# Kernel tuning notes

Hardware: AMD Instinct MI355X
Metric: run time of the kernel (lower is better)

Reference implementation:

```python
import jax, jax.numpy as jnp
import numpy as np

ATOM, BOND, INNER, HID, REC, OHID = 14, 3, 20, 34, 20, 25
N_NODES = 1048576
N_EDGES = 983040
MAX_DEPTH = 16
N_GRAPHS = 16384


def leaky(x):
    return jnp.where(x >= 0, x, 0.01 * x)


def setup_inputs() -> dict:
    key = jax.random.key(0)
    ks = jax.random.split(key, 20)
    p = 0.02
    atom_feats = jax.random.normal(ks[0], (N_NODES, ATOM), jnp.float32)
    bond_feats = jax.random.normal(ks[1], (N_EDGES, BOND), jnp.float32)
    # build a forest: node i's parent is some node with strictly smaller depth.
    # For a jit-friendly synthetic instance we assign depths and connect each
    # non-root node (edge) from a parent at depth d to child at depth d+1.
    depth = np.asarray(jax.random.randint(ks[2], (N_NODES,), 0, MAX_DEPTH))
    order = np.argsort(depth, kind='stable')
    depth_sorted = depth[order]
    # edges: child must have depth >= 1; pick children among nodes with depth>0
    child_pool = order[depth_sorted > 0]
    rng = np.random.default_rng(0)
    child_idx = rng.choice(child_pool, size=N_EDGES, replace=False) if len(child_pool) >= N_EDGES else rng.choice(child_pool, size=N_EDGES, replace=True)
    child_depth = depth[child_idx]
    # parent: random node with depth == child_depth - 1
    # bucket nodes by depth
    buckets = [order[depth_sorted == d] for d in range(MAX_DEPTH)]
    parent_idx = np.empty(N_EDGES, dtype=np.int64)
    for d in range(1, MAX_DEPTH):
        m = child_depth == d
        if m.sum() > 0:
            parent_idx[m] = rng.choice(buckets[d - 1], size=int(m.sum()))
    graph_id = np.asarray(jax.random.randint(ks[3], (N_NODES,), 0, N_GRAPHS))
    # roots: nodes with no incoming edge (not a child)
    is_child = np.zeros(N_NODES, dtype=bool)
    is_child[child_idx] = True
    is_root = (~is_child).astype(np.float32)
    params = {
        'inner_w': jax.random.normal(ks[4], (REC + BOND, INNER), jnp.float32) * p,
        'inner_b': jnp.zeros((INNER,), jnp.float32),
        'net_w1': jax.random.normal(ks[5], (INNER + ATOM, HID), jnp.float32) * p,
        'net_b1': jnp.zeros((HID,), jnp.float32),
        'net_w2': jax.random.normal(ks[6], (HID, REC), jnp.float32) * p,
        'net_b2': jnp.zeros((REC,), jnp.float32),
        'net0_w1': jax.random.normal(ks[7], (ATOM, HID), jnp.float32) * p,
        'net0_b1': jnp.zeros((HID,), jnp.float32),
        'net0_w2': jax.random.normal(ks[8], (HID, REC), jnp.float32) * p,
        'net0_b2': jnp.zeros((REC,), jnp.float32),
        'out_w1': jax.random.normal(ks[9], (REC, OHID), jnp.float32) * p,
        'out_b1': jnp.zeros((OHID,), jnp.float32),
        'out_w2': jax.random.normal(ks[10], (OHID, 1), jnp.float32) * p,
        'out_b2': jnp.zeros((1,), jnp.float32),
    }
    return dict(atom_feats=atom_feats, bond_feats=bond_feats,
                parent_idx=jnp.asarray(parent_idx), child_idx=jnp.asarray(child_idx),
                node_depth=jnp.asarray(depth), graph_id=jnp.asarray(graph_id),
                is_root=jnp.asarray(is_root), **params)


def reference(atom_feats, bond_feats, parent_idx, child_idx, node_depth, graph_id,
              is_root, inner_w, inner_b, net_w1, net_b1, net_w2, net_b2,
              net0_w1, net0_b1, net0_w2, net0_b2, out_w1, out_b1, out_w2, out_b2):
    n_nodes = atom_feats.shape[0]
    has_child = jnp.zeros((n_nodes,), jnp.float32).at[parent_idx].add(1.0) > 0
    # leaf vector via net0
    leaf_vec = leaky(leaky(atom_feats @ net0_w1 + net0_b1) @ net0_w2 + net0_b2)  # [N, REC]
    h = leaf_vec  # node recursive vectors; internal nodes filled bottom-up
    # process depths from deepest-1 parents up to 0: at step d, update nodes at depth d
    for d in range(MAX_DEPTH - 2, -1, -1):
        child_h = h[child_idx]  # [E, REC]
        msg = leaky(jnp.concatenate([bond_feats, child_h], axis=1) @ inner_w + inner_b)  # [E, INNER]
        # only edges whose parent is at depth d contribute this step
        edge_mask = (node_depth[parent_idx] == d).astype(msg.dtype)[:, None]
        inner_sum = jnp.zeros((n_nodes, INNER), msg.dtype).at[parent_idx].add(msg * edge_mask)
        x = jnp.concatenate([atom_feats, inner_sum], axis=1)  # [N, ATOM+INNER]
        new_h = leaky(leaky(x @ net_w1 + net_b1) @ net_w2 + net_b2)
        upd = ((node_depth == d) & has_child).astype(h.dtype)[:, None]
        h = h * (1.0 - upd) + new_h * upd
    # sum root vectors per graph
    root_h = h * is_root[:, None]
    g = jax.ops.segment_sum(root_h, graph_id, num_segments=N_GRAPHS)  # [G, REC]
    out = jnp.tanh(g @ out_w1 + out_b1) @ out_w2 + out_b2  # [G, 1]
    return out.reshape(-1)
```

## Files before the change

kernel.cpp:

```cpp
#include <hip/hip_runtime.h>

#define ATOM  14
#define BOND  3
#define INNER 20
#define HID   34
#define HIDP  36
#define REC   20
#define OHID  25
#define NN    1048576
#define NE    983040
#define NG    16384

#define NB    512
#define NT    256
#define GT    (NB*NT)
#define NIT   (NN/GT)

#define NB2   1024
#define NT2   256
#define NGRP  (NT2/4)
#define SSTR  (NGRP+1)
#define NBINS (NB2*32)

__device__ __forceinline__ float leaky(float x) { return x >= 0.f ? x : 0.01f * x; }

__device__ __forceinline__ void wsync() {
    __builtin_amdgcn_wave_barrier();
    __builtin_amdgcn_sched_barrier(0);
}

__device__ __forceinline__ void gbar_f(int* bar, int goal) {
    __syncthreads();
    if (threadIdx.x == 0) {
        __threadfence();
        __hip_atomic_fetch_add(bar, 1, __ATOMIC_RELEASE, __HIP_MEMORY_SCOPE_AGENT);
        while (__hip_atomic_load(bar, __ATOMIC_RELAXED, __HIP_MEMORY_SCOPE_AGENT) < goal)
            __builtin_amdgcn_s_sleep(32);
        __threadfence();
    }
    __syncthreads();
}

__global__ void k_pre(int* cnt_n, int2* pnode2, float* g, int* bin_cnt, int* totals, int* bars) {
    int tid = blockIdx.x * 256 + threadIdx.x;
    for (int i = tid; i < NN; i += 262144) { cnt_n[i] = 0; pnode2[i] = make_int2(i, -1); }
    for (int i = tid; i < NG * REC; i += 262144) g[i] = 0.f;
    for (int i = tid; i < NBINS; i += 262144) bin_cnt[i] = 0;
    if (tid == 0) { totals[0] = 0; totals[16] = 0; }
    if (tid == 1) for (int k = 0; k < 32; ++k) bars[k] = 0;
}

__global__ __launch_bounds__(NT) void k_prep(
    const int* __restrict__ parent, const int* __restrict__ child,
    const int* __restrict__ depth, const int* __restrict__ gid,
    const float* __restrict__ isr,
    int* cnt_n, int2* pnode2, int* K_s,
    int4* nodeinfo, int* row_n, int* adjc,
    int* bin_cnt, int* bin_base, int* bin_cur,
    int* totals, int* bar)
{
    __shared__ int sh[NT];
    __shared__ int sbase_sh;
    const int t = threadIdx.x;
    const int tid = blockIdx.x * NT + t;
    int ep = 0;

    for (int e = tid; e < NE; e += GT) {
        int p = parent[e];
        int r = atomicAdd(&cnt_n[p], 1);
        pnode2[child[e]] = make_int2(p, (r << 20) | e);
    }
    gbar_f(bar, NB * ++ep);

    for (int i = tid; i < NN; i += GT) {
        int d = depth[i];
        int r = i;
        for (int s = 0; s < d; ++s) r = pnode2[r].x;
        int K = (r & (NB2 - 1)) * 32 + d * 2 + (cnt_n[i] == 0 ? 1 : 0);
        K_s[i] = K;
        atomicAdd(&bin_cnt[K], 1);
    }
    gbar_f(bar, NB * ++ep);

    if (blockIdx.x < NBINS / NT) {
        int k0 = blockIdx.x * NT + t;
        int v = bin_cnt[k0];
        sh[t] = v;
        __syncthreads();
        for (int ofs = 1; ofs < NT; ofs <<= 1) {
            int x = (t >= ofs) ? sh[t - ofs] : 0;
            __syncthreads();
            sh[t] += x;
            __syncthreads();
        }
        if (t == NT - 1) sbase_sh = atomicAdd(&totals[0], sh[t]);
        __syncthreads();
        int b = sbase_sh + sh[t] - v;
        bin_base[k0] = b;
        bin_cur[k0] = b;
    }
    gbar_f(bar, NB * ++ep);

    for (int k = 0; k < NIT; ++k) {
        int i = tid + k * GT;
        int cn = cnt_n[i];
        __syncthreads();
        sh[t] = cn;
        __syncthreads();
        for (int ofs = 1; ofs < NT; ofs <<= 1) {
            int x = (t >= ofs) ? sh[t - ofs] : 0;
            __syncthreads();
            sh[t] += x;
            __syncthreads();
        }
        if (t == NT - 1) sbase_sh = atomicAdd(&totals[16], sh[t]);
        __syncthreads();
        int row = sbase_sh + sh[t] - cn;
        int pos = atomicAdd(&bin_cur[K_s[i]], 1);
        int2 pe = pnode2[i];
        int gr = (isr[i] != 0.f) ? gid[i] : -1;
        nodeinfo[pos] = make_int4(i, pe.y, gr, (row << 12) | cn);
        row_n[i] = row;
    }
    gbar_f(bar, NB * ++ep);

    for (int pos = tid; pos < NN; pos += GT) {
        int4 ni = nodeinfo[pos];
        if (ni.z < 0) {
            int ppn = pnode2[ni.x].x;
            int rank = ((unsigned)ni.y) >> 20;
            int slot = row_n[ppn] + rank;
            adjc[slot] = pos;
        }
    }
}

__device__ __forceinline__ void coop_mlp(int slot, int j, int KN,
                                         const float* xs, float* hs, float* os,
                                         const float* w1, const float* b1,
                                         const float* w2, const float* b2,
                                         float* o)
{
    wsync();
    float acc[9];
    #pragma unroll
    for (int u = 0; u < 9; ++u) { int h = 9*j + u; acc[u] = (h < HID) ? b1[h] : 0.f; }
    #pragma unroll 2
    for (int k = 0; k < KN; ++k) {
        float xk = xs[k * SSTR + slot];
        #pragma unroll
        for (int u = 0; u < 9; ++u) { int h = 9*j + u; if (h < HID) acc[u] += xk * w1[k * HIDP + h]; }
    }
    #pragma unroll
    for (int u = 0; u < 9; ++u) { int h = 9*j + u; if (h < HID) hs[h * SSTR + slot] = leaky(acc[u]); }
    wsync();
    #pragma unroll
    for (int u = 0; u < 5; ++u) o[u] = b2[5*j + u];
    #pragma unroll 2
    for (int k = 0; k < HID; ++k) {
        float hk = hs[k * SSTR + slot];
        #pragma unroll
        for (int u = 0; u < 5; ++u) o[u] += hk * w2[k * REC + 5*j + u];
    }
    #pragma unroll
    for (int u = 0; u < 5; ++u) { o[u] = leaky(o[u]); os[(5*j + u) * SSTR + slot] = o[u]; }
    wsync();
}

__global__ __launch_bounds__(NT2) void k_levels(
    const float* __restrict__ atom, const float* __restrict__ bond,
    const int4* __restrict__ nodeinfo, const int* __restrict__ adjc,
    const int* __restrict__ bin_base, const int* __restrict__ bin_cnt,
    const float* __restrict__ iw, const float* __restrict__ ib,
    const float* __restrict__ nw1, const float* __restrict__ nb1,
    const float* __restrict__ nw2, const float* __restrict__ nb2,
    const float* __restrict__ l0w1, const float* __restrict__ l0b1,
    const float* __restrict__ l0w2, const float* __restrict__ l0b2,
    float* __restrict__ g, float* __restrict__ msg_s)
{
    __shared__ float lw1[34 * HIDP];
    __shared__ float lw2[HID * REC];
    __shared__ float liw[23 * REC];
    __shared__ float zw1[ATOM * HIDP];
    __shared__ float zw2[HID * REC];
    __shared__ float lb1[HID], lb2[REC], lbi[INNER], zb1[HID], zb2[REC];
    __shared__ float xs[34 * SSTR];
    __shared__ float hs[34 * SSTR];
    __shared__ float os[20 * SSTR];

    const int t = threadIdx.x;
    const int b = blockIdx.x;
    const int slot = t >> 2;
    const int j = t & 3;

    for (int idx = t; idx < 34 * HIDP; idx += NT2) {
        int r = idx / HIDP, c = idx - r * HIDP;
        lw1[idx] = (c < HID) ? nw1[r * HID + c] : 0.f;
    }
    for (int idx = t; idx < HID * REC; idx += NT2) { lw2[idx] = nw2[idx]; zw2[idx] = l0w2[idx]; }
    for (int idx = t; idx < 23 * REC; idx += NT2) liw[idx] = iw[idx];
    for (int idx = t; idx < ATOM * HIDP; idx += NT2) {
        int r = idx / HIDP, c = idx - r * HIDP;
        zw1[idx] = (c < HID) ? l0w1[r * HID + c] : 0.f;
    }
    if (t < HID) { lb1[t] = nb1[t]; zb1[t] = l0b1[t]; }
    else if (t >= 64 && t < 64 + REC) { lb2[t - 64] = nb2[t - 64]; zb2[t - 64] = l0b2[t - 64]; }
    if (t >= 96 && t < 96 + INNER) lbi[t - 96] = ib[t - 96];
    __syncthreads();

    for (int d = 15; d >= 0; --d) {
        {
            int K = b * 32 + d * 2;
            int base = bin_base[K], n0 = bin_cnt[K];
            for (int idx = slot; idx < n0; idx += NGRP) {
                int pos = base + idx;
                int4 ni = nodeinfo[pos];
                int n   = ni.w & 0xFFF;
                int rp0 = ((unsigned)ni.w) >> 12;
                float s0 = 0.f, s1 = 0.f, s2 = 0.f, s3 = 0.f, s4 = 0.f;
                for (int r = rp0; r < rp0 + n; ++r) {
                    const float* mp = msg_s + (size_t)adjc[r] * REC + 5*j;
                    s0 += mp[0]; s1 += mp[1]; s2 += mp[2]; s3 += mp[3]; s4 += mp[4];
                }
                const float* ar = atom + (size_t)ni.x * ATOM;
                #pragma unroll
                for (int u = 0; u < 4; ++u) { int k = 4*j + u; if (k < ATOM) xs[k * SSTR + slot] = ar[k]; }
                xs[(ATOM + 5*j + 0) * SSTR + slot] = s0;
                xs[(ATOM + 5*j + 1) * SSTR + slot] = s1;
                xs[(ATOM + 5*j + 2) * SSTR + slot] = s2;
                xs[(ATOM + 5*j + 3) * SSTR + slot] = s3;
                xs[(ATOM + 5*j + 4) * SSTR + slot] = s4;
                float o[5];
                coop_mlp(slot, j, ATOM + INNER, xs, hs, os, lw1, lb1, lw2, lb2, o);
                if (ni.z >= 0) {
                    #pragma unroll
                    for (int u = 0; u < 5; ++u) atomicAdd(&g[(size_t)ni.z * REC + 5*j + u], o[u]);
                } else {
                    const float* br = bond + (size_t)(ni.y & 0xFFFFF) * BOND;
                    float b0 = br[0], b1 = br[1], b2 = br[2];
                    float m[5];
                    #pragma unroll
                    for (int u = 0; u < 5; ++u)
                        m[u] = lbi[5*j + u] + b0 * liw[0 * INNER + 5*j + u]
                             + b1 * liw[1 * INNER + 5*j + u] + b2 * liw[2 * INNER + 5*j + u];
                    #pragma unroll 2
                    for (int k = 0; k < REC; ++k) {
                        float ok = os[k * SSTR + slot];
                        #pragma unroll
                        for (int u = 0; u < 5; ++u) m[u] += ok * liw[(BOND + k) * INNER + 5*j + u];
                    }
                    #pragma unroll
                    for (int u = 0; u < 5; ++u) msg_s[(size_t)pos * REC + 5*j + u] = leaky(m[u]);
                }
            }
        }
        {
            int K = b * 32 + d * 2 + 1;
            int base = bin_base[K], n1 = bin_cnt[K];
            for (int idx = slot; idx < n1; idx += NGRP) {
                int pos = base + idx;
                int4 ni = nodeinfo[pos];
                const float* ar = atom + (size_t)ni.x * ATOM;
                #pragma unroll
                for (int u = 0; u < 4; ++u) { int k = 4*j + u; if (k < ATOM) xs[k * SSTR + slot] = ar[k]; }
                float o[5];
                coop_mlp(slot, j, ATOM, xs, hs, os, zw1, zb1, zw2, zb2, o);
                if (ni.z >= 0) {
                    #pragma unroll
                    for (int u = 0; u < 5; ++u) atomicAdd(&g[(size_t)ni.z * REC + 5*j + u], o[u]);
                } else {
                    const float* br = bond + (size_t)(ni.y & 0xFFFFF) * BOND;
                    float b0 = br[0], b1 = br[1], b2 = br[2];
                    float m[5];
                    #pragma unroll
                    for (int u = 0; u < 5; ++u)
                        m[u] = lbi[5*j + u] + b0 * liw[0 * INNER + 5*j + u]
                             + b1 * liw[1 * INNER + 5*j + u] + b2 * liw[2 * INNER + 5*j + u];
                    #pragma unroll 2
                    for (int k = 0; k < REC; ++k) {
                        float ok = os[k * SSTR + slot];
                        #pragma unroll
                        for (int u = 0; u < 5; ++u) m[u] += ok * liw[(BOND + k) * INNER + 5*j + u];
                    }
                    #pragma unroll
                    for (int u = 0; u < 5; ++u) msg_s[(size_t)pos * REC + 5*j + u] = leaky(m[u]);
                }
            }
        }
        __threadfence_block();
        __syncthreads();
    }
}

__global__ void k_out(const float* __restrict__ g,
                      const float* __restrict__ w1, const float* __restrict__ b1,
                      const float* __restrict__ w2, const float* __restrict__ b2,
                      float* __restrict__ out) {
    int t = blockIdx.x * 256 + threadIdx.x;
    if (t >= NG) return;
    const float* gv = g + (size_t)t * REC;
    float gl[REC];
    #pragma unroll
    for (int k = 0; k < REC; ++k) gl[k] = gv[k];
    float acc = b2[0];
    for (int j = 0; j < OHID; ++j) {
        float s = b1[j];
        #pragma unroll
        for (int k = 0; k < REC; ++k) s += gl[k] * w1[k * OHID + j];
        acc += tanhf(s) * w2[j];
    }
    out[t] = acc;
}

extern "C" void kernel_launch(void* const* d_in, const int* in_sizes, int n_in,
                              void* d_out, int out_size, void* d_ws, size_t ws_size,
                              hipStream_t stream) {
    const float* atom    = (const float*)d_in[0];
    const float* bond    = (const float*)d_in[1];
    const int*   parent  = (const int*)d_in[2];
    const int*   child   = (const int*)d_in[3];
    const int*   depth   = (const int*)d_in[4];
    const int*   gid     = (const int*)d_in[5];
    const float* isr     = (const float*)d_in[6];
    const float* inner_w = (const float*)d_in[7];
    const float* inner_b = (const float*)d_in[8];
    const float* net_w1  = (const float*)d_in[9];
    const float* net_b1  = (const float*)d_in[10];
    const float* net_w2  = (const float*)d_in[11];
    const float* net_b2  = (const float*)d_in[12];
    const float* net0_w1 = (const float*)d_in[13];
    const float* net0_b1 = (const float*)d_in[14];
    const float* net0_w2 = (const float*)d_in[15];
    const float* net0_b2 = (const float*)d_in[16];
    const float* out_w1  = (const float*)d_in[17];
    const float* out_b1  = (const float*)d_in[18];
    const float* out_w2  = (const float*)d_in[19];
    const float* out_b2  = (const float*)d_in[20];
    float* out = (float*)d_out;

    char* ws = (char*)d_ws;
    size_t o = 0;
    float* msg_s    = (float*)(ws + o);  o += (size_t)NN * REC * 4;
    int4* nodeinfo  = (int4*)(ws + o);   o += (size_t)NN * 16;
    float* g        = (float*)(ws + o);  o += (size_t)NG * REC * 4;
    int2* pnode2    = (int2*)(ws + o);   o += (size_t)NN * 8;
    int* adjc       = (int*)(ws + o);    o += (size_t)NE * 4;
    int* cnt_n      = (int*)(ws + o);    o += (size_t)NN * 4;
    int* row_n      = (int*)(ws + o);    o += (size_t)NN * 4;
    int* K_s        = (int*)(ws + o);    o += (size_t)NN * 4;
    int* bin_cnt    = (int*)(ws + o);    o += (size_t)NBINS * 4;
    int* bin_base   = (int*)(ws + o);    o += (size_t)NBINS * 4;
    int* bin_cur    = (int*)(ws + o);    o += (size_t)NBINS * 4;
    int* totals     = (int*)(ws + o);    o += 32 * 4;
    int* bars       = (int*)(ws + o);    o += 32 * 4;

    k_pre<<<1024, 256, 0, stream>>>(cnt_n, pnode2, g, bin_cnt, totals, bars);
    k_prep<<<NB, NT, 0, stream>>>(parent, child, depth, gid, isr,
                                  cnt_n, pnode2, K_s, nodeinfo, row_n,
                                  adjc, bin_cnt, bin_base, bin_cur, totals, bars);
    k_levels<<<NB2, NT2, 0, stream>>>(atom, bond, nodeinfo, adjc,
                                      bin_base, bin_cnt,
                                      inner_w, inner_b, net_w1, net_b1, net_w2, net_b2,
                                      net0_w1, net0_b1, net0_w2, net0_b2,
                                      g, msg_s);
    k_out<<<(NG + 255) / 256, 256, 0, stream>>>(g, out_w1, out_b1, out_w2, out_b2, out);
}
```

Before: 894.8 us.

## Store child messages in parent-contiguous rows instead of gather via adjacency

Child messages are now written straight into a CSR-ordered buffer at the slot their parent will read. Each parent then sums a contiguous run of message rows instead of gathering through an adjacency index. Row offsets are computed in sorted node order, so each bin's parents get neighbouring CSR rows. This costs an extra prep pass and grid barrier, plus inv/row_pos/slot_c arrays, and message writes become scattered.

```diff
diff --git a/kernel.cpp b/kernel.cpp
--- a/kernel.cpp
+++ b/kernel.cpp
@@ -54,8 +54,8 @@
     const int* __restrict__ parent, const int* __restrict__ child,
     const int* __restrict__ depth, const int* __restrict__ gid,
     const float* __restrict__ isr,
-    int* cnt_n, int2* pnode2, int* K_s,
-    int4* nodeinfo, int* row_n, int* adjc,
+    int* cnt_n, int2* pnode2, int* K_s, int* inv,
+    int4* nodeinfo, int* row_pos, int* slot_c,
     int* bin_cnt, int* bin_base, int* bin_cur,
     int* totals, int* bar)
 {
@@ -101,9 +101,18 @@
     }
     gbar_f(bar, NB * ++ep);
 
+    for (int i = tid; i < NN; i += GT) {
+        int pos = atomicAdd(&bin_cur[K_s[i]], 1);
+        int2 pe = pnode2[i];
+        int gr = (isr[i] != 0.f) ? gid[i] : -1;
+        nodeinfo[pos] = make_int4(i, pe.y, gr, cnt_n[i]);
+        inv[i] = pos;
+    }
+    gbar_f(bar, NB * ++ep);
+
     for (int k = 0; k < NIT; ++k) {
-        int i = tid + k * GT;
-        int cn = cnt_n[i];
+        int pos = tid + k * GT;
+        int cn = nodeinfo[pos].w;
         __syncthreads();
         sh[t] = cn;
         __syncthreads();
@@ -115,22 +124,17 @@
         }
         if (t == NT - 1) sbase_sh = atomicAdd(&totals[16], sh[t]);
         __syncthreads();
-        int row = sbase_sh + sh[t] - cn;
-        int pos = atomicAdd(&bin_cur[K_s[i]], 1);
-        int2 pe = pnode2[i];
-        int gr = (isr[i] != 0.f) ? gid[i] : -1;
-        nodeinfo[pos] = make_int4(i, pe.y, gr, (row << 12) | cn);
-        row_n[i] = row;
+        row_pos[pos] = sbase_sh + sh[t] - cn;
     }
     gbar_f(bar, NB * ++ep);
 
     for (int pos = tid; pos < NN; pos += GT) {
         int4 ni = nodeinfo[pos];
         if (ni.z < 0) {
-            int ppn = pnode2[ni.x].x;
+            int ppn  = pnode2[ni.x].x;
+            int ppos = inv[ppn];
             int rank = ((unsigned)ni.y) >> 20;
-            int slot = row_n[ppn] + rank;
-            adjc[slot] = pos;
+            slot_c[pos] = row_pos[ppos] + rank;
         }
     }
 }
@@ -169,14 +173,15 @@
 
 __global__ __launch_bounds__(NT2) void k_levels(
     const float* __restrict__ atom, const float* __restrict__ bond,
-    const int4* __restrict__ nodeinfo, const int* __restrict__ adjc,
+    const int4* __restrict__ nodeinfo, const int* __restrict__ row_pos,
+    const int* __restrict__ slot_c,
     const int* __restrict__ bin_base, const int* __restrict__ bin_cnt,
     const float* __restrict__ iw, const float* __restrict__ ib,
     const float* __restrict__ nw1, const float* __restrict__ nb1,
     const float* __restrict__ nw2, const float* __restrict__ nb2,
     const float* __restrict__ l0w1, const float* __restrict__ l0b1,
     const float* __restrict__ l0w2, const float* __restrict__ l0b2,
-    float* __restrict__ g, float* __restrict__ msg_s)
+    float* __restrict__ g, float* __restrict__ msg_row)
 {
     __shared__ float lw1[34 * HIDP];
     __shared__ float lw2[HID * REC];
@@ -215,11 +220,11 @@
             for (int idx = slot; idx < n0; idx += NGRP) {
                 int pos = base + idx;
                 int4 ni = nodeinfo[pos];
-                int n   = ni.w & 0xFFF;
-                int rp0 = ((unsigned)ni.w) >> 12;
+                int n   = ni.w;
+                int row = row_pos[pos];
                 float s0 = 0.f, s1 = 0.f, s2 = 0.f, s3 = 0.f, s4 = 0.f;
-                for (int r = rp0; r < rp0 + n; ++r) {
-                    const float* mp = msg_s + (size_t)adjc[r] * REC + 5*j;
+                const float* mp = msg_row + (size_t)row * REC + 5*j;
+                for (int r = 0; r < n; ++r, mp += REC) {
                     s0 += mp[0]; s1 += mp[1]; s2 += mp[2]; s3 += mp[3]; s4 += mp[4];
                 }
                 const float* ar = atom + (size_t)ni.x * ATOM;
@@ -249,8 +254,9 @@
                         #pragma unroll
                         for (int u = 0; u < 5; ++u) m[u] += ok * liw[(BOND + k) * INNER + 5*j + u];
                     }
-                    #pragma unroll
-                    for (int u = 0; u < 5; ++u) msg_s[(size_t)pos * REC + 5*j + u] = leaky(m[u]);
+                    float* mw = msg_row + (size_t)slot_c[pos] * REC + 5*j;
+                    #pragma unroll
+                    for (int u = 0; u < 5; ++u) mw[u] = leaky(m[u]);
                 }
             }
         }
@@ -282,8 +288,9 @@
                         #pragma unroll
                         for (int u = 0; u < 5; ++u) m[u] += ok * liw[(BOND + k) * INNER + 5*j + u];
                     }
-                    #pragma unroll
-                    for (int u = 0; u < 5; ++u) msg_s[(size_t)pos * REC + 5*j + u] = leaky(m[u]);
+                    float* mw = msg_row + (size_t)slot_c[pos] * REC + 5*j;
+                    #pragma unroll
+                    for (int u = 0; u < 5; ++u) mw[u] = leaky(m[u]);
                 }
             }
         }
@@ -340,13 +347,14 @@
 
     char* ws = (char*)d_ws;
     size_t o = 0;
-    float* msg_s    = (float*)(ws + o);  o += (size_t)NN * REC * 4;
+    float* msg_row  = (float*)(ws + o);  o += (size_t)NE * REC * 4;
     int4* nodeinfo  = (int4*)(ws + o);   o += (size_t)NN * 16;
     float* g        = (float*)(ws + o);  o += (size_t)NG * REC * 4;
     int2* pnode2    = (int2*)(ws + o);   o += (size_t)NN * 8;
-    int* adjc       = (int*)(ws + o);    o += (size_t)NE * 4;
     int* cnt_n      = (int*)(ws + o);    o += (size_t)NN * 4;
-    int* row_n      = (int*)(ws + o);    o += (size_t)NN * 4;
+    int* inv        = (int*)(ws + o);    o += (size_t)NN * 4;
+    int* row_pos    = (int*)(ws + o);    o += (size_t)NN * 4;
+    int* slot_c     = (int*)(ws + o);    o += (size_t)NN * 4;
     int* K_s        = (int*)(ws + o);    o += (size_t)NN * 4;
     int* bin_cnt    = (int*)(ws + o);    o += (size_t)NBINS * 4;
     int* bin_base   = (int*)(ws + o);    o += (size_t)NBINS * 4;
@@ -356,12 +364,12 @@
 
     k_pre<<<1024, 256, 0, stream>>>(cnt_n, pnode2, g, bin_cnt, totals, bars);
     k_prep<<<NB, NT, 0, stream>>>(parent, child, depth, gid, isr,
-                                  cnt_n, pnode2, K_s, nodeinfo, row_n,
-                                  adjc, bin_cnt, bin_base, bin_cur, totals, bars);
-    k_levels<<<NB2, NT2, 0, stream>>>(atom, bond, nodeinfo, adjc,
+                                  cnt_n, pnode2, K_s, inv, nodeinfo, row_pos,
+                                  slot_c, bin_cnt, bin_base, bin_cur, totals, bars);
+    k_levels<<<NB2, NT2, 0, stream>>>(atom, bond, nodeinfo, row_pos, slot_c,
                                       bin_base, bin_cnt,
                                       inner_w, inner_b, net_w1, net_b1, net_w2, net_b2,
                                       net0_w1, net0_b1, net0_w2, net0_b2,
-                                      g, msg_s);
+                                      g, msg_row);
     k_out<<<(NG + 255) / 256, 256, 0, stream>>>(g, out_w1, out_b1, out_w2, out_b2, out);
 }
```

New measurement: 967.2 us. 8.1% more time.
